# Kernel tuning notes

Measured on AMD Instinct MI355X. Metric: run time of the kernel, lower is better.

## Reference

```python
import jax, jax.numpy as jnp
import numpy as np

# ---- Mamba2 / model hyperparameters (from init_kwargs + mamba_ssm defaults) ----
D_MODEL = 64
D_STATE = 64
D_CONV = 4
EXPAND = 2
HEADDIM = 64                      # mamba_ssm Mamba2 default
D_INNER = EXPAND * D_MODEL        # 128
NHEADS = D_INNER // HEADDIM       # 2
CONV_DIM = D_INNER + 2 * D_STATE  # 256 (ngroups=1)
D_IN_PROJ = 2 * D_INNER + 2 * D_STATE + NHEADS  # 386
B, T, F_ = 4, 128, 128
EPS = 1e-5


def silu(x):
    return x * jax.nn.sigmoid(x)


def depthwise_causal_conv(x, w, b):
    # x: [N, L, C], w: [C, K], b: [C]  (causal depthwise conv, as in Mamba2)
    xt = x.transpose(0, 2, 1)           # [N, C, L]
    kernel = w[:, None, :]              # [C, 1, K]
    y = jax.lax.conv_general_dilated(
        xt, kernel, window_strides=(1,), padding=[(D_CONV - 1, 0)],
        feature_group_count=CONV_DIM)
    return y.transpose(0, 2, 1) + b     # [N, L, C]


def mamba2(u, Wp, cw, cb, dtb, Al, Dp, nw, Wo):
    # u: [N, L, D_MODEL]
    Nb, L, _ = u.shape
    zxbcdt = u @ Wp.T                                   # [N, L, D_IN_PROJ]
    z = zxbcdt[..., :D_INNER]
    xBC = zxbcdt[..., D_INNER:D_INNER + CONV_DIM]
    dt = jax.nn.softplus(zxbcdt[..., -NHEADS:] + dtb)   # [N, L, H]
    xBC = silu(depthwise_causal_conv(xBC, cw, cb))
    x = xBC[..., :D_INNER].reshape(Nb, L, NHEADS, HEADDIM)
    Bm = xBC[..., D_INNER:D_INNER + D_STATE]            # [N, L, Nst]
    Cm = xBC[..., D_INNER + D_STATE:]                   # [N, L, Nst]
    dA = jnp.exp(dt * (-jnp.exp(Al)))                   # [N, L, H]

    def step(h, inp):
        # h: [N, H, P, Nst]
        dA_t, dt_t, x_t, B_t, C_t = inp
        h = h * dA_t[:, :, None, None] + (dt_t[:, :, None] * x_t)[..., None] * B_t[:, None, None, :]
        y = jnp.einsum('bhpn,bn->bhp', h, C_t)
        return h, y

    h0 = jnp.zeros((Nb, NHEADS, HEADDIM, D_STATE), u.dtype)
    xs = (dA.transpose(1, 0, 2), dt.transpose(1, 0, 2),
          x.transpose(1, 0, 2, 3), Bm.transpose(1, 0, 2), Cm.transpose(1, 0, 2))
    _, ys = jax.lax.scan(step, h0, xs)                  # ys: [L, N, H, P]
    y = ys.transpose(1, 0, 2, 3) + Dp[None, None, :, None] * x
    y = y.reshape(Nb, L, D_INNER)
    # RMSNormGated (norm_before_gate=False): gate then rms-normalize
    g = y * silu(z)
    g = g * jax.lax.rsqrt(jnp.mean(g * g, axis=-1, keepdims=True) + EPS) * nw
    return g @ Wo.T                                     # [N, L, D_MODEL]


def bimamba(u, p_fwd, p_bwd, fW, fb):
    out_f = mamba2(u, *p_fwd)
    out_b = mamba2(u[:, ::-1], *p_bwd)[:, ::-1]
    return jnp.concatenate([out_f, out_b], axis=-1) @ fW.T + fb


def layernorm(x, w, b):
    m = jnp.mean(x, axis=-1, keepdims=True)
    v = jnp.mean((x - m) ** 2, axis=-1, keepdims=True)
    return (x - m) * jax.lax.rsqrt(v + EPS) * w + b


def setup_inputs() -> dict:
    key = jax.random.key(0)
    ks = jax.random.split(key, 12)
    inp = {
        'x': jax.random.normal(ks[0], (B, D_MODEL, T, F_), jnp.float32),
        # 4 Mamba2 instances stacked: [freq_fwd, freq_bwd, time_fwd, time_bwd]
        'in_proj_W': 0.02 * jax.random.normal(ks[1], (4, D_IN_PROJ, D_MODEL), jnp.float32),
        'conv_W': 0.1 * jax.random.normal(ks[2], (4, CONV_DIM, D_CONV), jnp.float32),
        'conv_b': jnp.zeros((4, CONV_DIM), jnp.float32),
        'dt_bias': 0.1 * jax.random.normal(ks[3], (4, NHEADS), jnp.float32),
        'A_log': jnp.log(jax.random.uniform(ks[4], (4, NHEADS), jnp.float32, 1.0, 16.0)),
        'D_param': 0.1 * jax.random.normal(ks[5], (4, NHEADS), jnp.float32),
        'norm_w': jnp.ones((4, D_INNER), jnp.float32),
        'out_W': 0.02 * jax.random.normal(ks[6], (4, D_MODEL, D_INNER), jnp.float32),
        # 2 BiMamba fusion linears: [freq, time]
        'fusion_W': 0.02 * jax.random.normal(ks[7], (2, D_MODEL, 2 * D_MODEL), jnp.float32),
        'fusion_b': jnp.zeros((2, D_MODEL), jnp.float32),
        # 2 LayerNorms: [freq, time]
        'ln_w': jnp.ones((2, D_MODEL), jnp.float32),
        'ln_b': jnp.zeros((2, D_MODEL), jnp.float32),
    }
    return inp


def reference(x, in_proj_W, conv_W, conv_b, dt_bias, A_log, D_param, norm_w, out_W,
              fusion_W, fusion_b, ln_w, ln_b):
    Bb, Cc, Tt, Ff = x.shape

    def mp(i):
        return (in_proj_W[i], conv_W[i], conv_b[i], dt_bias[i], A_log[i],
                D_param[i], norm_w[i], out_W[i])

    # ---- frequency axis scan (dilation == 1) ----
    x_freq = x.transpose(0, 2, 3, 1).reshape(Bb * Tt, Ff, Cc)
    xf_out = bimamba(layernorm(x_freq, ln_w[0], ln_b[0]), mp(0), mp(1), fusion_W[0], fusion_b[0])
    x = x + xf_out.reshape(Bb, Tt, Ff, Cc).transpose(0, 3, 1, 2)

    # ---- time axis scan ----
    x_time = x.transpose(0, 3, 2, 1).reshape(Bb * Ff, Tt, Cc)
    xt_out = bimamba(layernorm(x_time, ln_w[1], ln_b[1]), mp(2), mp(3), fusion_W[1], fusion_b[1])
    x = x + xt_out.reshape(Bb, Ff, Tt, Cc).transpose(0, 3, 2, 1)
    return x
```

## Files before the change

### kernel.cpp

```cpp
#include <hip/hip_runtime.h>

#define EPSV 1e-5f

typedef short bf16x8 __attribute__((ext_vector_type(8)));
typedef float f32x4 __attribute__((ext_vector_type(4)));

__device__ __forceinline__ float sigmoidf_(float x) {
  return 1.f / (1.f + __expf(-x));
}
__device__ __forceinline__ unsigned short f2bf(float f) {
  unsigned int u = __float_as_uint(f);
  u += 0x7fffu + ((u >> 16) & 1u);
  return (unsigned short)(u >> 16);
}
__device__ __forceinline__ float bfu(unsigned short h) {
  union { unsigned int u; float f; } t; t.u = ((unsigned int)h) << 16; return t.f;
}
__device__ __forceinline__ float bflo(unsigned int u) {
  union { unsigned int x; float f; } t; t.x = u << 16; return t.f;
}
__device__ __forceinline__ float bfhi(unsigned int u) {
  union { unsigned int x; float f; } t; t.x = u & 0xffff0000u; return t.f;
}

__global__ __launch_bounds__(256) void precomp_wc(
    const float* __restrict__ fW,
    const float* __restrict__ oW,
    float* __restrict__ Wc)
{
  const int bi = blockIdx.x;
  const int i = bi >> 3, mg = bi & 7;
  const int m = (mg << 3) + (threadIdx.x >> 5);
  const int k0 = (threadIdx.x & 31) << 2;
  const int p = i >> 1, d = i & 1;
  const float* fr = fW + p * 8192 + m * 128 + d * 64;
  const float* orow = oW + i * 8192 + k0;
  float a0 = 0.f, a1 = 0.f, a2 = 0.f, a3 = 0.f;
  for (int j = 0; j < 64; ++j) {
    const float f = fr[j];
    const float4 o4 = *(const float4*)(orow + j * 128);
    a0 += f * o4.x; a1 += f * o4.y; a2 += f * o4.z; a3 += f * o4.w;
  }
  float* out = Wc + i * 8192 + m * 128 + k0;
  out[0] = a0; out[1] = a1; out[2] = a2; out[3] = a3;
}

__global__ __launch_bounds__(256) void precomp_wcf(
    const float* __restrict__ Wc, unsigned short* __restrict__ WcF)
{
  const int ip = blockIdx.x;
  const float* src = Wc + (size_t)ip * 8192;
  unsigned short* dst = WcF + (size_t)ip * 8192;
  for (int idx = threadIdx.x; idx < 8192; idx += 256) {
    const int tile = idx >> 11;
    const int h = (idx >> 9) & 3;
    const int lane = (idx >> 3) & 63;
    const int j = idx & 7;
    const int col = lane & 15, quad = lane >> 4;
    dst[idx] = f2bf(src[(tile * 16 + col) * 128 + h * 32 + quad * 8 + j]);
  }
}

__global__ __launch_bounds__(256) void precomp_wpf(
    const float* __restrict__ Wp, unsigned short* __restrict__ WpF)
{
  const int ip = blockIdx.x;
  const float* src = Wp + (size_t)ip * 24704;
  unsigned short* dst = WpF + (size_t)ip * 25600;
  for (int idx = threadIdx.x; idx < 25600; idx += 256) {
    const int tile = idx >> 10;
    const int rem = idx & 1023;
    const int h = rem >> 9;
    const int lane = (rem >> 3) & 63;
    const int j = idx & 7;
    const int col = lane & 15, quad = lane >> 4;
    const int o = tile * 16 + col;
    const int k = h * 32 + quad * 8 + j;
    dst[idx] = (o < 386) ? f2bf(src[o * 64 + k]) : (unsigned short)0;
  }
}

__global__ __launch_bounds__(256) void transp0(
    const float* __restrict__ x, float* __restrict__ x0)
{
  __shared__ float T[64 * 132];
  const int tid = threadIdx.x, blk = blockIdx.x;
  const int b = blk >> 7, t = blk & 127;
  {
    const int c = tid >> 2, f0 = (tid & 3) << 5;
    const float* xp = x + (((size_t)(b * 64 + c) * 128 + t) << 7) + f0;
    float* tp = &T[c * 132 + f0];
    #pragma unroll
    for (int j = 0; j < 8; ++j)
      *(float4*)(tp + (j << 2)) = *(const float4*)(xp + (j << 2));
  }
  __syncthreads();
  {
    const int f = tid >> 1, cb = (tid & 1) << 5;
    float* op = x0 + (((size_t)(b * 128 + t) * 128 + f) << 6) + cb;
    #pragma unroll
    for (int j = 0; j < 32; j += 4) {
      float4 v;
      v.x = T[(cb + j + 0) * 132 + f];
      v.y = T[(cb + j + 1) * 132 + f];
      v.z = T[(cb + j + 2) * 132 + f];
      v.w = T[(cb + j + 3) * 132 + f];
      *(float4*)(op + j) = v;
    }
  }
}

__global__ __launch_bounds__(512, 4) void mamba_dir(
    const float* __restrict__ src,
    unsigned short* __restrict__ ybuf,
    const unsigned short* __restrict__ WpF,
    const unsigned short* __restrict__ WcF,
    const float* __restrict__ cwA, const float* __restrict__ cbA,
    const float* __restrict__ dtbA, const float* __restrict__ AlA,
    const float* __restrict__ DpA, const float* __restrict__ nwA,
    const float* __restrict__ lnwA, const float* __restrict__ lnbA,
    int phase)
{
  __shared__ __align__(16) unsigned short sU[16 * 72];
  __shared__ __align__(16) unsigned short sZb[16 * 136];
  __shared__ __align__(16) float sZx[16 * 260];
  __shared__ __align__(16) unsigned short sBC16[16 * 136];
  __shared__ __align__(16) unsigned short sXdT[128 * 40];
  __shared__ __align__(16) unsigned short sXwT[128 * 40];
  __shared__ __align__(16) unsigned short sBT[64 * 40];
  __shared__ __align__(16) unsigned short sSm[2 * 16 * 40];
  __shared__ __align__(16) unsigned short sH[2 * 64 * 72];
  __shared__ float sMeta[16][2][4];
  __shared__ float sDtRaw[16][2];

  const int tid = threadIdx.x;
  const int blk = blockIdx.x;
  const int seq = blk >> 1, dir = blk & 1;
  const int ip = (phase << 1) + dir;
  const float dtb0 = dtbA[ip * 2], dtb1 = dtbA[ip * 2 + 1];
  const float nA0 = -__expf(AlA[ip * 2]), nA1 = -__expf(AlA[ip * 2 + 1]);
  const float Dp0 = DpA[ip * 2], Dp1 = DpA[ip * 2 + 1];
  const int c256 = tid & 255;
  const int lh = tid >> 8;
  const float4 cw4 = *(const float4*)(cwA + ip * 1024 + (c256 << 2));
  const float cbias = cbA[ip * 256 + c256];
  float ch0 = 0.f, ch1 = 0.f, ch2 = 0.f;

  const int wv = tid >> 6, lane = tid & 63;
  const int col = lane & 15, quad = lane >> 4;

  f32x4 hacc[8];
  #pragma unroll
  for (int i = 0; i < 8; ++i) hacc[i] = (f32x4){0.f, 0.f, 0.f, 0.f};

  {
    unsigned int* z;
    z = (unsigned int*)sXdT; for (int i = tid; i < 2560; i += 512) z[i] = 0u;
    z = (unsigned int*)sXwT; for (int i = tid; i < 2560; i += 512) z[i] = 0u;
    z = (unsigned int*)sBT;  for (int i = tid; i < 1280; i += 512) z[i] = 0u;
    z = (unsigned int*)sSm;  for (int i = tid; i < 640;  i += 512) z[i] = 0u;
    z = (unsigned int*)sH;   for (int i = tid; i < 4608; i += 512) z[i] = 0u;
  }

  const unsigned short* wf = WpF + (size_t)ip * 25600;
  const unsigned short* wcf = WcF + (size_t)ip * 8192;
  const size_t sb = (size_t)seq << 13;
  const int pos = tid >> 6, lc = tid & 63;
  const int lnb_i = (phase << 6) + lc;
  const float lnw_v = lnwA[lnb_i], lnb_v = lnbA[lnb_i];

  float vc0, vc1;
  {
    const int p0 = dir ? (127 - pos) : pos;
    const int p1 = dir ? (127 - (pos + 8)) : (pos + 8);
    vc0 = src[sb + (size_t)p0 * 64 + lc];
    vc1 = src[sb + (size_t)p1 * 64 + lc];
  }

  for (int ck = 0; ck < 8; ++ck) {
    float vn0 = 0.f, vn1 = 0.f;
    if (ck < 7) {
      const int st0 = ((ck + 1) << 4) + pos;
      const int p0 = dir ? (127 - st0) : st0;
      const int p1 = dir ? (127 - (st0 + 8)) : (st0 + 8);
      vn0 = src[sb + (size_t)p0 * 64 + lc];
      vn1 = src[sb + (size_t)p1 * 64 + lc];
    }
    #pragma unroll
    for (int half = 0; half < 2; ++half) {
      const float v = half ? vc1 : vc0;
      float sm = v, s2 = v * v;
      sm += __shfl_xor(sm, 1);  s2 += __shfl_xor(s2, 1);
      sm += __shfl_xor(sm, 2);  s2 += __shfl_xor(s2, 2);
      sm += __shfl_xor(sm, 4);  s2 += __shfl_xor(s2, 4);
      sm += __shfl_xor(sm, 8);  s2 += __shfl_xor(s2, 8);
      sm += __shfl_xor(sm, 16); s2 += __shfl_xor(s2, 16);
      sm += __shfl_xor(sm, 32); s2 += __shfl_xor(s2, 32);
      const float mean = sm * (1.f / 64.f);
      const float inv = rsqrtf(s2 * (1.f / 64.f) - mean * mean + EPSV);
      sU[(pos + half * 8) * 72 + lc] = f2bf((v - mean) * inv * lnw_v + lnb_v);
    }
    __syncthreads();
    {
      const int wave = tid >> 6;
      const bf16x8 a0 = *(const bf16x8*)(&sU[col * 72 + quad * 8]);
      const bf16x8 a1 = *(const bf16x8*)(&sU[col * 72 + quad * 8 + 32]);
      for (int tile = wave; tile < 25; tile += 8) {
        const unsigned short* wt = wf + (tile << 10) + (lane << 3);
        const bf16x8 b0 = *(const bf16x8*)(wt);
        const bf16x8 b1 = *(const bf16x8*)(wt + 512);
        f32x4 d = {0.f, 0.f, 0.f, 0.f};
        d = __builtin_amdgcn_mfma_f32_16x16x32_bf16(a0, b0, d, 0, 0, 0);
        d = __builtin_amdgcn_mfma_f32_16x16x32_bf16(a1, b1, d, 0, 0, 0);
        const int o = (tile << 4) + col;
        if (tile < 8) {
          #pragma unroll
          for (int r = 0; r < 4; ++r)
            sZb[(quad * 4 + r) * 136 + o] = f2bf(d[r]);
        } else if (tile < 24) {
          #pragma unroll
          for (int r = 0; r < 4; ++r)
            sZx[(quad * 4 + r) * 260 + (o - 128)] = d[r];
        } else if (col < 2) {
          #pragma unroll
          for (int r = 0; r < 4; ++r)
            sDtRaw[quad * 4 + r][col] = d[r];
        }
      }
    }
    __syncthreads();
    {
      const int c = c256;
      float a0c, a1c, a2c;
      if (lh == 0) { a0c = ch0; a1c = ch1; a2c = ch2; }
      else {
        a0c = sZx[5 * 260 + c];
        a1c = sZx[6 * 260 + c];
        a2c = sZx[7 * 260 + c];
      }
      const int lt0 = lh << 3;
      unsigned int pkv[4];
      #pragma unroll
      for (int l = 0; l < 8; ++l) {
        const int lt = lt0 + l;
        const float a3 = sZx[lt * 260 + c];
        const float acc = cbias + a0c * cw4.x + a1c * cw4.y + a2c * cw4.z + a3 * cw4.w;
        const float sv = acc * sigmoidf_(acc);
        const unsigned int hv = (unsigned int)f2bf(sv);
        if (c >= 192)      sBC16[lt * 136 + 64 + (c - 192)] = (unsigned short)hv;
        else if (c >= 128) sBC16[lt * 136 + (c - 128)] = (unsigned short)hv;
        if (l & 1) pkv[l >> 1] |= hv << 16; else pkv[l >> 1] = hv;
        a0c = a1c; a1c = a2c; a2c = a3;
      }
      if (c < 128)
        *(uint4*)(&sXdT[c * 40 + lt0]) = make_uint4(pkv[0], pkv[1], pkv[2], pkv[3]);
      else if (c < 192)
        *(uint4*)(&sBT[(c - 128) * 40 + lt0]) = make_uint4(pkv[0], pkv[1], pkv[2], pkv[3]);
      if (lh == 0) {
        ch0 = sZx[13 * 260 + c];
        ch1 = sZx[14 * 260 + c];
        ch2 = sZx[15 * 260 + c];
      }
      if (tid < 32) {
        const int lt = tid >> 1, hh = tid & 1;
        const float rawv = sDtRaw[lt][hh] + (hh ? dtb1 : dtb0);
        const float dtv = (rawv > 20.f) ? rawv : log1pf(__expf(rawv));
        float Lx = dtv * (hh ? nA1 : nA0);
        #pragma unroll
        for (int d = 2; d < 32; d <<= 1) {
          const float tpv = __shfl_up(Lx, d);
          Lx += (tid >= d) ? tpv : 0.f;
        }
        const float Ltot = __shfl(Lx, 30 + hh);
        *(float4*)(&sMeta[lt][hh][0]) =
            make_float4(Lx, dtv, __expf(Ltot - Lx) * dtv, __expf(Lx));
      }
    }
    __syncthreads();
    f32x4 yD0, yD1;
    if (wv == 0) {
      const bf16x8 ca0 = *(const bf16x8*)(&sBC16[col * 136 + 64 + quad * 8]);
      const bf16x8 ca1 = *(const bf16x8*)(&sBC16[col * 136 + 96 + quad * 8]);
      const bf16x8 bb0 = *(const bf16x8*)(&sBC16[col * 136 + quad * 8]);
      const bf16x8 bb1 = *(const bf16x8*)(&sBC16[col * 136 + 32 + quad * 8]);
      f32x4 g = {0.f, 0.f, 0.f, 0.f};
      g = __builtin_amdgcn_mfma_f32_16x16x32_bf16(ca0, bb0, g, 0, 0, 0);
      g = __builtin_amdgcn_mfma_f32_16x16x32_bf16(ca1, bb1, g, 0, 0, 0);
      #pragma unroll
      for (int h = 0; h < 2; ++h) {
        const float Ls = sMeta[col][h][0];
        const float dts = sMeta[col][h][1];
        #pragma unroll
        for (int r = 0; r < 4; ++r) {
          const int t = quad * 4 + r;
          const float m = (col <= t) ? __expf(sMeta[t][h][0] - Ls) * dts : 0.f;
          sSm[(h * 16 + t) * 40 + col] = f2bf(g[r] * m);
        }
      }
    } else if (wv <= 2) {
      if (ck < 7) {
        const int p = ((wv - 1) << 6) + lane;
        const int hh = p >> 6;
        #pragma unroll
        for (int tp = 0; tp < 8; ++tp) {
          const unsigned int xr = *(const unsigned int*)(&sXdT[p * 40 + tp * 2]);
          const unsigned int lo = (unsigned int)f2bf(bflo(xr) * sMeta[tp * 2][hh][2]);
          const unsigned int hi = (unsigned int)f2bf(bfhi(xr) * sMeta[tp * 2 + 1][hh][2]);
          *(unsigned int*)(&sXwT[p * 40 + tp * 2]) = lo | (hi << 16);
        }
      }
    } else if (wv >= 4) {
      const int h = (wv - 4) >> 1, pt2 = (wv - 4) & 1;
      const bf16x8 ca0 = *(const bf16x8*)(&sBC16[col * 136 + 64 + quad * 8]);
      const bf16x8 ca1 = *(const bf16x8*)(&sBC16[col * 136 + 96 + quad * 8]);
      const unsigned short* hp0 = &sH[(h * 64 + pt2 * 32 + col) * 72];
      const unsigned short* hp1 = hp0 + 16 * 72;
      const bf16x8 h00 = *(const bf16x8*)(hp0 + quad * 8);
      const bf16x8 h01 = *(const bf16x8*)(hp0 + 32 + quad * 8);
      const bf16x8 h10 = *(const bf16x8*)(hp1 + quad * 8);
      const bf16x8 h11 = *(const bf16x8*)(hp1 + 32 + quad * 8);
      yD0 = (f32x4){0.f, 0.f, 0.f, 0.f};
      yD1 = (f32x4){0.f, 0.f, 0.f, 0.f};
      yD0 = __builtin_amdgcn_mfma_f32_16x16x32_bf16(ca0, h00, yD0, 0, 0, 0);
      yD0 = __builtin_amdgcn_mfma_f32_16x16x32_bf16(ca1, h01, yD0, 0, 0, 0);
      yD1 = __builtin_amdgcn_mfma_f32_16x16x32_bf16(ca0, h10, yD1, 0, 0, 0);
      yD1 = __builtin_amdgcn_mfma_f32_16x16x32_bf16(ca1, h11, yD1, 0, 0, 0);
      #pragma unroll
      for (int r = 0; r < 4; ++r) {
        const float Pv = sMeta[quad * 4 + r][h][3];
        yD0[r] *= Pv; yD1[r] *= Pv;
      }
    }
    __syncthreads();
    if (wv < 4) {
      if (ck < 7) {
        const int h = wv >> 1, ph = wv & 1;
        const int pb = h * 64 + ph * 32;
        const float At = sMeta[15][h][3];
        const bf16x8 xa0 = *(const bf16x8*)(&sXwT[(pb + col) * 40 + quad * 8]);
        const bf16x8 xa1 = *(const bf16x8*)(&sXwT[(pb + 16 + col) * 40 + quad * 8]);
        #pragma unroll
        for (int nt = 0; nt < 4; ++nt) {
          const bf16x8 bbt = *(const bf16x8*)(&sBT[(nt * 16 + col) * 40 + quad * 8]);
          #pragma unroll
          for (int r = 0; r < 4; ++r) { hacc[nt][r] *= At; hacc[nt + 4][r] *= At; }
          hacc[nt]     = __builtin_amdgcn_mfma_f32_16x16x32_bf16(xa0, bbt, hacc[nt], 0, 0, 0);
          hacc[nt + 4] = __builtin_amdgcn_mfma_f32_16x16x32_bf16(xa1, bbt, hacc[nt + 4], 0, 0, 0);
        }
        #pragma unroll
        for (int nt = 0; nt < 4; ++nt) {
          #pragma unroll
          for (int r = 0; r < 4; ++r) {
            sH[(pb + quad * 4 + r) * 72 + nt * 16 + col] = f2bf(hacc[nt][r]);
            sH[(pb + 16 + quad * 4 + r) * 72 + nt * 16 + col] = f2bf(hacc[nt + 4][r]);
          }
        }
      }
    } else {
      const int h = (wv - 4) >> 1, pt2 = (wv - 4) & 1;
      const int cb0 = h * 64 + pt2 * 32;
      const float dp = h ? Dp1 : Dp0;
      const bf16x8 sa = *(const bf16x8*)(&sSm[(h * 16 + col) * 40 + quad * 8]);
      const bf16x8 xb0 = *(const bf16x8*)(&sXdT[(cb0 + col) * 40 + quad * 8]);
      const bf16x8 xb1 = *(const bf16x8*)(&sXdT[(cb0 + 16 + col) * 40 + quad * 8]);
      yD0 = __builtin_amdgcn_mfma_f32_16x16x32_bf16(sa, xb0, yD0, 0, 0, 0);
      yD1 = __builtin_amdgcn_mfma_f32_16x16x32_bf16(sa, xb1, yD1, 0, 0, 0);
      const uint2 xw0 = *(const uint2*)(&sXdT[(cb0 + col) * 40 + quad * 4]);
      const uint2 xw1 = *(const uint2*)(&sXdT[(cb0 + 16 + col) * 40 + quad * 4]);
      yD0[0] += dp * bflo(xw0.x); yD0[1] += dp * bfhi(xw0.x);
      yD0[2] += dp * bflo(xw0.y); yD0[3] += dp * bfhi(xw0.y);
      yD1[0] += dp * bflo(xw1.x); yD1[1] += dp * bfhi(xw1.x);
      yD1[2] += dp * bflo(xw1.y); yD1[3] += dp * bfhi(xw1.y);
      #pragma unroll
      for (int r = 0; r < 4; ++r) {
        sZx[(quad * 4 + r) * 260 + cb0 + col] = yD0[r];
        sZx[(quad * 4 + r) * 260 + cb0 + 16 + col] = yD1[r];
      }
    }
    __syncthreads();
    {
      const int w = tid >> 6, kk = tid & 63, k0 = kk << 1;
      #pragma unroll
      for (int sub = 0; sub < 2; ++sub) {
        const int lt = w + (sub << 3);
        const float2 yv = *(const float2*)(&sZx[lt * 260 + k0]);
        const unsigned int zp = *(const unsigned int*)(&sZb[lt * 136 + k0]);
        const float z0 = bflo(zp), z1 = bfhi(zp);
        const float g0 = yv.x * (z0 * sigmoidf_(z0));
        const float g1 = yv.y * (z1 * sigmoidf_(z1));
        float ssq = g0 * g0 + g1 * g1;
        ssq += __shfl_xor(ssq, 1);
        ssq += __shfl_xor(ssq, 2);
        ssq += __shfl_xor(ssq, 4);
        ssq += __shfl_xor(ssq, 8);
        ssq += __shfl_xor(ssq, 16);
        ssq += __shfl_xor(ssq, 32);
        const float sc = rsqrtf(ssq * (1.f / 128.f) + EPSV);
        const float2 nw2 = *(const float2*)(nwA + ip * 128 + k0);
        const unsigned int lo = f2bf(g0 * sc * nw2.x);
        const unsigned int hi = f2bf(g1 * sc * nw2.y);
        *(unsigned int*)(&sZb[lt * 136 + k0]) = lo | (hi << 16);
      }
    }
    __syncthreads();
    {
      const int wave = tid >> 6;
      if (wave < 4) {
        const unsigned short* wt = wcf + (wave << 11);
        f32x4 d = {0.f, 0.f, 0.f, 0.f};
        #pragma unroll
        for (int h = 0; h < 4; ++h) {
          const bf16x8 a = *(const bf16x8*)(&sZb[col * 136 + (h << 5) + (quad << 3)]);
          const bf16x8 bb = *(const bf16x8*)(wt + (h << 9) + (lane << 3));
          d = __builtin_amdgcn_mfma_f32_16x16x32_bf16(a, bb, d, 0, 0, 0);
        }
        const size_t yb = ((size_t)(dir * 512 + seq) * 128) << 6;
        #pragma unroll
        for (int r = 0; r < 4; ++r) {
          const int pp = (quad << 2) + r;
          const int st = (ck << 4) + pp, rp = dir ? (127 - st) : st;
          ybuf[yb + ((size_t)rp << 6) + (wave << 4) + col] = f2bf(d[r]);
        }
      }
    }
    vc0 = vn0; vc1 = vn1;
  }
}

__global__ __launch_bounds__(256) void combine0(
    const float* __restrict__ x, const unsigned short* __restrict__ ybuf,
    const float* __restrict__ fb, float* __restrict__ x1)
{
  __shared__ float T[64 * 132];
  const int tid = threadIdx.x, blk = blockIdx.x;
  const int b = blk >> 7, t = blk & 127;
  {
    const int c = tid >> 2, f0 = (tid & 3) << 5;
    const float* xp = x + (((size_t)(b * 64 + c) * 128 + t) << 7) + f0;
    float* tp = &T[c * 132 + f0];
    #pragma unroll
    for (int j = 0; j < 8; ++j)
      *(float4*)(tp + (j << 2)) = *(const float4*)(xp + (j << 2));
  }
  __syncthreads();
  {
    const int f = tid >> 1, cb = (tid & 1) << 5;
    const size_t s0 = (size_t)b * 128 + t;
    const unsigned short* yf = ybuf + ((s0 * 128 + f) << 6) + cb;
    const unsigned short* yb = ybuf + (((s0 + 512) * 128 + f) << 6) + cb;
    float* op = x1 + (((size_t)(b * 128 + f) * 128 + t) << 6) + cb;
    #pragma unroll
    for (int j = 0; j < 32; j += 4) {
      float4 v;
      v.x = T[(cb + j + 0) * 132 + f] + bfu(yf[j + 0]) + bfu(yb[j + 0]) + fb[cb + j + 0];
      v.y = T[(cb + j + 1) * 132 + f] + bfu(yf[j + 1]) + bfu(yb[j + 1]) + fb[cb + j + 1];
      v.z = T[(cb + j + 2) * 132 + f] + bfu(yf[j + 2]) + bfu(yb[j + 2]) + fb[cb + j + 2];
      v.w = T[(cb + j + 3) * 132 + f] + bfu(yf[j + 3]) + bfu(yb[j + 3]) + fb[cb + j + 3];
      *(float4*)(op + j) = v;
    }
  }
}

__global__ __launch_bounds__(256) void combine1(
    const float* __restrict__ x1, const unsigned short* __restrict__ ybuf,
    const float* __restrict__ fb, float* __restrict__ out)
{
  __shared__ float T[128 * 68];
  const int tid = threadIdx.x, blk = blockIdx.x;
  const int b = blk >> 7, t = blk & 127;
  {
    const int f = tid >> 1, cb = (tid & 1) << 5;
    const size_t s1 = (size_t)b * 128 + f;
    const float* xp = x1 + ((s1 * 128 + t) << 6) + cb;
    const unsigned short* yf = ybuf + ((s1 * 128 + t) << 6) + cb;
    const unsigned short* yb = ybuf + (((s1 + 512) * 128 + t) << 6) + cb;
    float* tp = &T[f * 68 + cb];
    #pragma unroll
    for (int j = 0; j < 32; ++j)
      tp[j] = xp[j] + bfu(yf[j]) + bfu(yb[j]) + fb[cb + j];
  }
  __syncthreads();
  {
    const int c = tid >> 2, f0 = (tid & 3) << 5;
    float* op = out + (((size_t)(b * 64 + c) * 128 + t) << 7) + f0;
    #pragma unroll
    for (int j = 0; j < 32; j += 4) {
      float4 v;
      v.x = T[(f0 + j + 0) * 68 + c];
      v.y = T[(f0 + j + 1) * 68 + c];
      v.z = T[(f0 + j + 2) * 68 + c];
      v.w = T[(f0 + j + 3) * 68 + c];
      *(float4*)(op + j) = v;
    }
  }
}

extern "C" void kernel_launch(void* const* d_in, const int* in_sizes, int n_in,
                              void* d_out, int out_size, void* d_ws, size_t ws_size,
                              hipStream_t stream) {
  const float* x   = (const float*)d_in[0];
  const float* Wp  = (const float*)d_in[1];
  const float* cw  = (const float*)d_in[2];
  const float* cb  = (const float*)d_in[3];
  const float* dtb = (const float*)d_in[4];
  const float* Al  = (const float*)d_in[5];
  const float* Dp  = (const float*)d_in[6];
  const float* nw  = (const float*)d_in[7];
  const float* oW  = (const float*)d_in[8];
  const float* fW  = (const float*)d_in[9];
  const float* fb  = (const float*)d_in[10];
  const float* lnw = (const float*)d_in[11];
  const float* lnb = (const float*)d_in[12];

  float* ws = (float*)d_ws;
  float* Wc = ws;
  unsigned short* WpF = (unsigned short*)(ws + 32768);
  unsigned short* WcF = (unsigned short*)(ws + 32768 + 51200);
  float* xbuf = ws + 32768 + 51200 + 16384;
  unsigned short* y = (unsigned short*)(xbuf + 4194304);

  precomp_wc<<<32, 256, 0, stream>>>(fW, oW, Wc);
  precomp_wcf<<<4, 256, 0, stream>>>(Wc, WcF);
  precomp_wpf<<<4, 256, 0, stream>>>(Wp, WpF);
  transp0<<<512, 256, 0, stream>>>(x, xbuf);
  mamba_dir<<<1024, 512, 0, stream>>>(xbuf, y, WpF, WcF, cw, cb, dtb, Al, Dp,
                                      nw, lnw, lnb, 0);
  combine0<<<512, 256, 0, stream>>>(x, y, fb, xbuf);
  mamba_dir<<<1024, 512, 0, stream>>>(xbuf, y, WpF, WcF, cw, cb, dtb, Al, Dp,
                                      nw, lnw, lnb, 1);
  combine1<<<512, 256, 0, stream>>>(xbuf, y, fb + 64, (float*)d_out);
}
```

Baseline: 398.5 us.

## Shrink Mamba scan LDS via aliasing, bf16 staging, and 16x16x16 MFMA

Reworks shared memory in the Mamba direction kernel. The raw projection buffer is stored as bf16, and it and the y buffer share one region, as do sU and sSm. The x/B transpose buffers are narrowed to 16-step rows. The intra-chunk MFMAs switch to the 16x16x16 bf16 form, so the zero-padded K=32 operands and their initialisation are no longer needed. The decay weighting moves from x onto B per head. Launch bounds drop to 3 blocks per SM. combine1 is vectorised with float4/uint2 loads. This removes zero-fill and LDS traffic, but adds bf16 rounding of the pre-conv activations.

```diff
diff --git a/kernel.cpp b/kernel.cpp
--- a/kernel.cpp
+++ b/kernel.cpp
@@ -3,6 +3,7 @@
 #define EPSV 1e-5f
 
 typedef short bf16x8 __attribute__((ext_vector_type(8)));
+typedef short bf16x4 __attribute__((ext_vector_type(4)));
 typedef float f32x4 __attribute__((ext_vector_type(4)));
 
 __device__ __forceinline__ float sigmoidf_(float x) {
@@ -22,6 +23,18 @@
 __device__ __forceinline__ float bfhi(unsigned int u) {
   union { unsigned int x; float f; } t; t.x = u & 0xffff0000u; return t.f;
 }
+
+#if __has_builtin(__builtin_amdgcn_mfma_f32_16x16x16bf16_1k)
+__device__ __forceinline__ f32x4 mfma16(bf16x4 a, bf16x4 b, f32x4 c) {
+  return __builtin_amdgcn_mfma_f32_16x16x16bf16_1k(a, b, c, 0, 0, 0);
+}
+#else
+__device__ __forceinline__ f32x4 mfma16(bf16x4 a, bf16x4 b, f32x4 c) {
+  bf16x8 a8 = {a[0], a[1], a[2], a[3], 0, 0, 0, 0};
+  bf16x8 b8 = {b[0], b[1], b[2], b[3], 0, 0, 0, 0};
+  return __builtin_amdgcn_mfma_f32_16x16x32_bf16(a8, b8, c, 0, 0, 0);
+}
+#endif
 
 __global__ __launch_bounds__(256) void precomp_wc(
     const float* __restrict__ fW,
@@ -110,7 +123,7 @@
   }
 }
 
-__global__ __launch_bounds__(512, 4) void mamba_dir(
+__global__ __launch_bounds__(512, 3) void mamba_dir(
     const float* __restrict__ src,
     unsigned short* __restrict__ ybuf,
     const unsigned short* __restrict__ WpF,
@@ -121,17 +134,20 @@
     const float* __restrict__ lnwA, const float* __restrict__ lnbA,
     int phase)
 {
-  __shared__ __align__(16) unsigned short sU[16 * 72];
+  __shared__ __align__(16) unsigned char u0[2304];
+  __shared__ __align__(16) unsigned char uXY[8448];
   __shared__ __align__(16) unsigned short sZb[16 * 136];
-  __shared__ __align__(16) float sZx[16 * 260];
   __shared__ __align__(16) unsigned short sBC16[16 * 136];
-  __shared__ __align__(16) unsigned short sXdT[128 * 40];
-  __shared__ __align__(16) unsigned short sXwT[128 * 40];
-  __shared__ __align__(16) unsigned short sBT[64 * 40];
-  __shared__ __align__(16) unsigned short sSm[2 * 16 * 40];
+  __shared__ __align__(16) unsigned short sXdT[128 * 24];
+  __shared__ __align__(16) unsigned short sBTw[2 * 64 * 24];
   __shared__ __align__(16) unsigned short sH[2 * 64 * 72];
   __shared__ float sMeta[16][2][4];
   __shared__ float sDtRaw[16][2];
+
+  unsigned short* sU   = (unsigned short*)u0;
+  unsigned short* sSm  = (unsigned short*)u0;
+  unsigned short* sRaw = (unsigned short*)uXY;
+  float*          sY   = (float*)uXY;
 
   const int tid = threadIdx.x;
   const int blk = blockIdx.x;
@@ -140,51 +156,45 @@
   const float dtb0 = dtbA[ip * 2], dtb1 = dtbA[ip * 2 + 1];
   const float nA0 = -__expf(AlA[ip * 2]), nA1 = -__expf(AlA[ip * 2 + 1]);
   const float Dp0 = DpA[ip * 2], Dp1 = DpA[ip * 2 + 1];
+
+  const int wv = tid >> 6, lane = tid & 63;
+  const int col = lane & 15, quad = lane >> 4;
+
   const int c256 = tid & 255;
   const int lh = tid >> 8;
+  const int lt0 = lh << 3;
   const float4 cw4 = *(const float4*)(cwA + ip * 1024 + (c256 << 2));
   const float cbias = cbA[ip * 256 + c256];
   float ch0 = 0.f, ch1 = 0.f, ch2 = 0.f;
 
-  const int wv = tid >> 6, lane = tid & 63;
-  const int col = lane & 15, quad = lane >> 4;
-
   f32x4 hacc[8];
   #pragma unroll
   for (int i = 0; i < 8; ++i) hacc[i] = (f32x4){0.f, 0.f, 0.f, 0.f};
 
-  {
-    unsigned int* z;
-    z = (unsigned int*)sXdT; for (int i = tid; i < 2560; i += 512) z[i] = 0u;
-    z = (unsigned int*)sXwT; for (int i = tid; i < 2560; i += 512) z[i] = 0u;
-    z = (unsigned int*)sBT;  for (int i = tid; i < 1280; i += 512) z[i] = 0u;
-    z = (unsigned int*)sSm;  for (int i = tid; i < 640;  i += 512) z[i] = 0u;
-    z = (unsigned int*)sH;   for (int i = tid; i < 4608; i += 512) z[i] = 0u;
-  }
-
   const unsigned short* wf = WpF + (size_t)ip * 25600;
   const unsigned short* wcf = WcF + (size_t)ip * 8192;
   const size_t sb = (size_t)seq << 13;
-  const int pos = tid >> 6, lc = tid & 63;
-  const int lnb_i = (phase << 6) + lc;
+  const int lnb_i = (phase << 6) + lane;
   const float lnw_v = lnwA[lnb_i], lnb_v = lnbA[lnb_i];
+  const int k0g = lane << 1;
+  const float2 nw2 = *(const float2*)(nwA + ip * 128 + k0g);
 
   float vc0, vc1;
   {
-    const int p0 = dir ? (127 - pos) : pos;
-    const int p1 = dir ? (127 - (pos + 8)) : (pos + 8);
-    vc0 = src[sb + (size_t)p0 * 64 + lc];
-    vc1 = src[sb + (size_t)p1 * 64 + lc];
+    const int p0 = dir ? (127 - wv) : wv;
+    const int p1 = dir ? (127 - (wv + 8)) : (wv + 8);
+    vc0 = src[sb + (size_t)p0 * 64 + lane];
+    vc1 = src[sb + (size_t)p1 * 64 + lane];
   }
 
   for (int ck = 0; ck < 8; ++ck) {
     float vn0 = 0.f, vn1 = 0.f;
     if (ck < 7) {
-      const int st0 = ((ck + 1) << 4) + pos;
+      const int st0 = ((ck + 1) << 4) + wv;
       const int p0 = dir ? (127 - st0) : st0;
       const int p1 = dir ? (127 - (st0 + 8)) : (st0 + 8);
-      vn0 = src[sb + (size_t)p0 * 64 + lc];
-      vn1 = src[sb + (size_t)p1 * 64 + lc];
+      vn0 = src[sb + (size_t)p0 * 64 + lane];
+      vn1 = src[sb + (size_t)p1 * 64 + lane];
     }
     #pragma unroll
     for (int half = 0; half < 2; ++half) {
@@ -198,14 +208,13 @@
       sm += __shfl_xor(sm, 32); s2 += __shfl_xor(s2, 32);
       const float mean = sm * (1.f / 64.f);
       const float inv = rsqrtf(s2 * (1.f / 64.f) - mean * mean + EPSV);
-      sU[(pos + half * 8) * 72 + lc] = f2bf((v - mean) * inv * lnw_v + lnb_v);
+      sU[(wv + half * 8) * 72 + lane] = f2bf((v - mean) * inv * lnw_v + lnb_v);
     }
     __syncthreads();
     {
-      const int wave = tid >> 6;
       const bf16x8 a0 = *(const bf16x8*)(&sU[col * 72 + quad * 8]);
       const bf16x8 a1 = *(const bf16x8*)(&sU[col * 72 + quad * 8 + 32]);
-      for (int tile = wave; tile < 25; tile += 8) {
+      for (int tile = wv; tile < 25; tile += 8) {
         const unsigned short* wt = wf + (tile << 10) + (lane << 3);
         const bf16x8 b0 = *(const bf16x8*)(wt);
         const bf16x8 b1 = *(const bf16x8*)(wt + 512);
@@ -220,7 +229,7 @@
         } else if (tile < 24) {
           #pragma unroll
           for (int r = 0; r < 4; ++r)
-            sZx[(quad * 4 + r) * 260 + (o - 128)] = d[r];
+            sRaw[(quad * 4 + r) * 264 + (o - 128)] = f2bf(d[r]);
         } else if (col < 2) {
           #pragma unroll
           for (int r = 0; r < 4; ++r)
@@ -234,36 +243,49 @@
       float a0c, a1c, a2c;
       if (lh == 0) { a0c = ch0; a1c = ch1; a2c = ch2; }
       else {
-        a0c = sZx[5 * 260 + c];
-        a1c = sZx[6 * 260 + c];
-        a2c = sZx[7 * 260 + c];
-      }
-      const int lt0 = lh << 3;
-      unsigned int pkv[4];
-      #pragma unroll
-      for (int l = 0; l < 8; ++l) {
-        const int lt = lt0 + l;
-        const float a3 = sZx[lt * 260 + c];
-        const float acc = cbias + a0c * cw4.x + a1c * cw4.y + a2c * cw4.z + a3 * cw4.w;
-        const float sv = acc * sigmoidf_(acc);
-        const unsigned int hv = (unsigned int)f2bf(sv);
-        if (c >= 192)      sBC16[lt * 136 + 64 + (c - 192)] = (unsigned short)hv;
-        else if (c >= 128) sBC16[lt * 136 + (c - 128)] = (unsigned short)hv;
-        if (l & 1) pkv[l >> 1] |= hv << 16; else pkv[l >> 1] = hv;
-        a0c = a1c; a1c = a2c; a2c = a3;
-      }
-      if (c < 128)
-        *(uint4*)(&sXdT[c * 40 + lt0]) = make_uint4(pkv[0], pkv[1], pkv[2], pkv[3]);
-      else if (c < 192)
-        *(uint4*)(&sBT[(c - 128) * 40 + lt0]) = make_uint4(pkv[0], pkv[1], pkv[2], pkv[3]);
+        a0c = bfu(sRaw[5 * 264 + c]);
+        a1c = bfu(sRaw[6 * 264 + c]);
+        a2c = bfu(sRaw[7 * 264 + c]);
+      }
+      if (c < 128) {
+        unsigned int prev = 0u;
+        #pragma unroll
+        for (int l = 0; l < 8; ++l) {
+          const int lt = lt0 + l;
+          const float a3 = bfu(sRaw[lt * 264 + c]);
+          const float acc = cbias + a0c * cw4.x + a1c * cw4.y + a2c * cw4.z + a3 * cw4.w;
+          const unsigned int hv = (unsigned int)f2bf(acc * sigmoidf_(acc));
+          if (l & 1) *(unsigned int*)(&sXdT[c * 24 + lt - 1]) = prev | (hv << 16);
+          else prev = hv;
+          a0c = a1c; a1c = a2c; a2c = a3;
+        }
+      } else if (c < 192) {
+        #pragma unroll
+        for (int l = 0; l < 8; ++l) {
+          const int lt = lt0 + l;
+          const float a3 = bfu(sRaw[lt * 264 + c]);
+          const float acc = cbias + a0c * cw4.x + a1c * cw4.y + a2c * cw4.z + a3 * cw4.w;
+          sBC16[lt * 136 + (c - 128)] = f2bf(acc * sigmoidf_(acc));
+          a0c = a1c; a1c = a2c; a2c = a3;
+        }
+      } else {
+        #pragma unroll
+        for (int l = 0; l < 8; ++l) {
+          const int lt = lt0 + l;
+          const float a3 = bfu(sRaw[lt * 264 + c]);
+          const float acc = cbias + a0c * cw4.x + a1c * cw4.y + a2c * cw4.z + a3 * cw4.w;
+          sBC16[lt * 136 + 64 + (c - 192)] = f2bf(acc * sigmoidf_(acc));
+          a0c = a1c; a1c = a2c; a2c = a3;
+        }
+      }
       if (lh == 0) {
-        ch0 = sZx[13 * 260 + c];
-        ch1 = sZx[14 * 260 + c];
-        ch2 = sZx[15 * 260 + c];
+        ch0 = bfu(sRaw[13 * 264 + c]);
+        ch1 = bfu(sRaw[14 * 264 + c]);
+        ch2 = bfu(sRaw[15 * 264 + c]);
       }
       if (tid < 32) {
-        const int lt = tid >> 1, hh = tid & 1;
-        const float rawv = sDtRaw[lt][hh] + (hh ? dtb1 : dtb0);
+        const int t = tid >> 1, hh = tid & 1;
+        const float rawv = sDtRaw[t][hh] + (hh ? dtb1 : dtb0);
         const float dtv = (rawv > 20.f) ? rawv : log1pf(__expf(rawv));
         float Lx = dtv * (hh ? nA1 : nA0);
         #pragma unroll
@@ -272,12 +294,12 @@
           Lx += (tid >= d) ? tpv : 0.f;
         }
         const float Ltot = __shfl(Lx, 30 + hh);
-        *(float4*)(&sMeta[lt][hh][0]) =
+        *(float4*)(&sMeta[t][hh][0]) =
             make_float4(Lx, dtv, __expf(Ltot - Lx) * dtv, __expf(Lx));
       }
     }
     __syncthreads();
-    f32x4 yD0, yD1;
+    f32x4 yAcc[2];
     if (wv == 0) {
       const bf16x8 ca0 = *(const bf16x8*)(&sBC16[col * 136 + 64 + quad * 8]);
       const bf16x8 ca1 = *(const bf16x8*)(&sBC16[col * 136 + 96 + quad * 8]);
@@ -294,58 +316,57 @@
         for (int r = 0; r < 4; ++r) {
           const int t = quad * 4 + r;
           const float m = (col <= t) ? __expf(sMeta[t][h][0] - Ls) * dts : 0.f;
-          sSm[(h * 16 + t) * 40 + col] = f2bf(g[r] * m);
+          sSm[h * 384 + t * 24 + col] = f2bf(g[r] * m);
         }
       }
     } else if (wv <= 2) {
-      if (ck < 7) {
-        const int p = ((wv - 1) << 6) + lane;
-        const int hh = p >> 6;
-        #pragma unroll
-        for (int tp = 0; tp < 8; ++tp) {
-          const unsigned int xr = *(const unsigned int*)(&sXdT[p * 40 + tp * 2]);
-          const unsigned int lo = (unsigned int)f2bf(bflo(xr) * sMeta[tp * 2][hh][2]);
-          const unsigned int hi = (unsigned int)f2bf(bfhi(xr) * sMeta[tp * 2 + 1][hh][2]);
-          *(unsigned int*)(&sXwT[p * 40 + tp * 2]) = lo | (hi << 16);
-        }
+      const int idx = tid - 64;
+      const int h = idx >> 6, n = idx & 63;
+      unsigned int prev = 0u;
+      #pragma unroll
+      for (int t = 0; t < 16; ++t) {
+        const float bv = bfu(sBC16[t * 136 + n]) * sMeta[t][h][2];
+        const unsigned int hv = (unsigned int)f2bf(bv);
+        if (t & 1) *(unsigned int*)(&sBTw[h * 1536 + n * 24 + t - 1]) = prev | (hv << 16);
+        else prev = hv;
       }
     } else if (wv >= 4) {
-      const int h = (wv - 4) >> 1, pt2 = (wv - 4) & 1;
-      const bf16x8 ca0 = *(const bf16x8*)(&sBC16[col * 136 + 64 + quad * 8]);
-      const bf16x8 ca1 = *(const bf16x8*)(&sBC16[col * 136 + 96 + quad * 8]);
-      const unsigned short* hp0 = &sH[(h * 64 + pt2 * 32 + col) * 72];
-      const unsigned short* hp1 = hp0 + 16 * 72;
-      const bf16x8 h00 = *(const bf16x8*)(hp0 + quad * 8);
-      const bf16x8 h01 = *(const bf16x8*)(hp0 + 32 + quad * 8);
-      const bf16x8 h10 = *(const bf16x8*)(hp1 + quad * 8);
-      const bf16x8 h11 = *(const bf16x8*)(hp1 + 32 + quad * 8);
-      yD0 = (f32x4){0.f, 0.f, 0.f, 0.f};
-      yD1 = (f32x4){0.f, 0.f, 0.f, 0.f};
-      yD0 = __builtin_amdgcn_mfma_f32_16x16x32_bf16(ca0, h00, yD0, 0, 0, 0);
-      yD0 = __builtin_amdgcn_mfma_f32_16x16x32_bf16(ca1, h01, yD0, 0, 0, 0);
-      yD1 = __builtin_amdgcn_mfma_f32_16x16x32_bf16(ca0, h10, yD1, 0, 0, 0);
-      yD1 = __builtin_amdgcn_mfma_f32_16x16x32_bf16(ca1, h11, yD1, 0, 0, 0);
-      #pragma unroll
-      for (int r = 0; r < 4; ++r) {
-        const float Pv = sMeta[quad * 4 + r][h][3];
-        yD0[r] *= Pv; yD1[r] *= Pv;
+      const int q = wv - 4, hq = q >> 1, ptp = (q & 1) << 1;
+      if (ck) {
+        const bf16x8 ca0 = *(const bf16x8*)(&sBC16[col * 136 + 64 + quad * 8]);
+        const bf16x8 ca1 = *(const bf16x8*)(&sBC16[col * 136 + 96 + quad * 8]);
+        #pragma unroll
+        for (int i = 0; i < 2; ++i) {
+          const int pt = ptp + i;
+          const unsigned short* hp = &sH[(hq * 64 + pt * 16 + col) * 72];
+          const bf16x8 h0 = *(const bf16x8*)(hp + quad * 8);
+          const bf16x8 h1 = *(const bf16x8*)(hp + 32 + quad * 8);
+          f32x4 d = {0.f, 0.f, 0.f, 0.f};
+          d = __builtin_amdgcn_mfma_f32_16x16x32_bf16(ca0, h0, d, 0, 0, 0);
+          d = __builtin_amdgcn_mfma_f32_16x16x32_bf16(ca1, h1, d, 0, 0, 0);
+          #pragma unroll
+          for (int r = 0; r < 4; ++r) d[r] *= sMeta[quad * 4 + r][hq][3];
+          yAcc[i] = d;
+        }
+      } else {
+        yAcc[0] = (f32x4){0.f, 0.f, 0.f, 0.f};
+        yAcc[1] = (f32x4){0.f, 0.f, 0.f, 0.f};
       }
     }
     __syncthreads();
     if (wv < 4) {
       if (ck < 7) {
-        const int h = wv >> 1, ph = wv & 1;
-        const int pb = h * 64 + ph * 32;
+        const int h = wv >> 1, pb = h * 64 + (wv & 1) * 32;
         const float At = sMeta[15][h][3];
-        const bf16x8 xa0 = *(const bf16x8*)(&sXwT[(pb + col) * 40 + quad * 8]);
-        const bf16x8 xa1 = *(const bf16x8*)(&sXwT[(pb + 16 + col) * 40 + quad * 8]);
+        const bf16x4 xa0 = *(const bf16x4*)(&sXdT[(pb + col) * 24 + quad * 4]);
+        const bf16x4 xa1 = *(const bf16x4*)(&sXdT[(pb + 16 + col) * 24 + quad * 4]);
         #pragma unroll
         for (int nt = 0; nt < 4; ++nt) {
-          const bf16x8 bbt = *(const bf16x8*)(&sBT[(nt * 16 + col) * 40 + quad * 8]);
+          const bf16x4 bb = *(const bf16x4*)(&sBTw[h * 1536 + (nt * 16 + col) * 24 + quad * 4]);
           #pragma unroll
           for (int r = 0; r < 4; ++r) { hacc[nt][r] *= At; hacc[nt + 4][r] *= At; }
-          hacc[nt]     = __builtin_amdgcn_mfma_f32_16x16x32_bf16(xa0, bbt, hacc[nt], 0, 0, 0);
-          hacc[nt + 4] = __builtin_amdgcn_mfma_f32_16x16x32_bf16(xa1, bbt, hacc[nt + 4], 0, 0, 0);
+          hacc[nt]     = mfma16(xa0, bb, hacc[nt]);
+          hacc[nt + 4] = mfma16(xa1, bb, hacc[nt + 4]);
         }
         #pragma unroll
         for (int nt = 0; nt < 4; ++nt) {
@@ -357,34 +378,28 @@
         }
       }
     } else {
-      const int h = (wv - 4) >> 1, pt2 = (wv - 4) & 1;
-      const int cb0 = h * 64 + pt2 * 32;
-      const float dp = h ? Dp1 : Dp0;
-      const bf16x8 sa = *(const bf16x8*)(&sSm[(h * 16 + col) * 40 + quad * 8]);
-      const bf16x8 xb0 = *(const bf16x8*)(&sXdT[(cb0 + col) * 40 + quad * 8]);
-      const bf16x8 xb1 = *(const bf16x8*)(&sXdT[(cb0 + 16 + col) * 40 + quad * 8]);
-      yD0 = __builtin_amdgcn_mfma_f32_16x16x32_bf16(sa, xb0, yD0, 0, 0, 0);
-      yD1 = __builtin_amdgcn_mfma_f32_16x16x32_bf16(sa, xb1, yD1, 0, 0, 0);
-      const uint2 xw0 = *(const uint2*)(&sXdT[(cb0 + col) * 40 + quad * 4]);
-      const uint2 xw1 = *(const uint2*)(&sXdT[(cb0 + 16 + col) * 40 + quad * 4]);
-      yD0[0] += dp * bflo(xw0.x); yD0[1] += dp * bfhi(xw0.x);
-      yD0[2] += dp * bflo(xw0.y); yD0[3] += dp * bfhi(xw0.y);
-      yD1[0] += dp * bflo(xw1.x); yD1[1] += dp * bfhi(xw1.x);
-      yD1[2] += dp * bflo(xw1.y); yD1[3] += dp * bfhi(xw1.y);
+      const int q = wv - 4, hq = q >> 1, ptp = (q & 1) << 1;
+      const float dp = hq ? Dp1 : Dp0;
+      const bf16x4 sa = *(const bf16x4*)(&sSm[hq * 384 + col * 24 + quad * 4]);
       #pragma unroll
-      for (int r = 0; r < 4; ++r) {
-        sZx[(quad * 4 + r) * 260 + cb0 + col] = yD0[r];
-        sZx[(quad * 4 + r) * 260 + cb0 + 16 + col] = yD1[r];
+      for (int i = 0; i < 2; ++i) {
+        const int c = hq * 64 + (ptp + i) * 16 + col;
+        const bf16x4 xb = *(const bf16x4*)(&sXdT[c * 24 + quad * 4]);
+        f32x4 y = mfma16(sa, xb, yAcc[i]);
+        #pragma unroll
+        for (int r = 0; r < 4; ++r) {
+          y[r] += dp * bfu((unsigned short)xb[r]);
+          sY[(quad * 4 + r) * 132 + c] = y[r];
+        }
       }
     }
     __syncthreads();
     {
-      const int w = tid >> 6, kk = tid & 63, k0 = kk << 1;
       #pragma unroll
       for (int sub = 0; sub < 2; ++sub) {
-        const int lt = w + (sub << 3);
-        const float2 yv = *(const float2*)(&sZx[lt * 260 + k0]);
-        const unsigned int zp = *(const unsigned int*)(&sZb[lt * 136 + k0]);
+        const int lt = wv + (sub << 3);
+        const float2 yv = *(const float2*)(&sY[lt * 132 + k0g]);
+        const unsigned int zp = *(const unsigned int*)(&sZb[lt * 136 + k0g]);
         const float z0 = bflo(zp), z1 = bfhi(zp);
         const float g0 = yv.x * (z0 * sigmoidf_(z0));
         const float g1 = yv.y * (z1 * sigmoidf_(z1));
@@ -396,17 +411,15 @@
         ssq += __shfl_xor(ssq, 16);
         ssq += __shfl_xor(ssq, 32);
         const float sc = rsqrtf(ssq * (1.f / 128.f) + EPSV);
-        const float2 nw2 = *(const float2*)(nwA + ip * 128 + k0);
         const unsigned int lo = f2bf(g0 * sc * nw2.x);
         const unsigned int hi = f2bf(g1 * sc * nw2.y);
-        *(unsigned int*)(&sZb[lt * 136 + k0]) = lo | (hi << 16);
+        *(unsigned int*)(&sZb[lt * 136 + k0g]) = lo | (hi << 16);
       }
     }
     __syncthreads();
     {
-      const int wave = tid >> 6;
-      if (wave < 4) {
-        const unsigned short* wt = wcf + (wave << 11);
+      if (wv < 4) {
+        const unsigned short* wt = wcf + (wv << 11);
         f32x4 d = {0.f, 0.f, 0.f, 0.f};
         #pragma unroll
         for (int h = 0; h < 4; ++h) {
@@ -417,9 +430,9 @@
         const size_t yb = ((size_t)(dir * 512 + seq) * 128) << 6;
         #pragma unroll
         for (int r = 0; r < 4; ++r) {
-          const int pp = (quad << 2) + r;
-          const int st = (ck << 4) + pp, rp = dir ? (127 - st) : st;
-          ybuf[yb + ((size_t)rp << 6) + (wave << 4) + col] = f2bf(d[r]);
+          const int st = (ck << 4) + (quad << 2) + r;
+          const int rp = dir ? (127 - st) : st;
+          ybuf[yb + ((size_t)rp << 6) + (wv << 4) + col] = f2bf(d[r]);
         }
       }
     }
@@ -476,8 +489,16 @@
     const unsigned short* yb = ybuf + (((s1 + 512) * 128 + t) << 6) + cb;
     float* tp = &T[f * 68 + cb];
     #pragma unroll
-    for (int j = 0; j < 32; ++j)
-      tp[j] = xp[j] + bfu(yf[j]) + bfu(yb[j]) + fb[cb + j];
+    for (int j = 0; j < 32; j += 4) {
+      const float4 xv = *(const float4*)(xp + j);
+      const uint2 yfv = *(const uint2*)(yf + j);
+      const uint2 ybv = *(const uint2*)(yb + j);
+      const float4 fv = *(const float4*)(fb + cb + j);
+      tp[j + 0] = xv.x + bflo(yfv.x) + bflo(ybv.x) + fv.x;
+      tp[j + 1] = xv.y + bfhi(yfv.x) + bfhi(ybv.x) + fv.y;
+      tp[j + 2] = xv.z + bflo(yfv.y) + bflo(ybv.y) + fv.z;
+      tp[j + 3] = xv.w + bfhi(yfv.y) + bfhi(ybv.y) + fv.w;
+    }
   }
   __syncthreads();
   {
```

Measured after the change: 474.8 us. +19.1%, slower.
